# Kernel optimization log

Hardware: AMD Instinct MI355X
Metric: run time of the kernel (lower is better)

The kernel has to match this reference:

```python
import jax, jax.numpy as jnp
import numpy as np

B, T, C, H, K = 4, 2048, 2048, 32, 64
CHUNK = 64  # matches `splits = 64` in the torch source
EPS = 0.00064


def setup_inputs() -> dict:
    key = jax.random.key(0)
    ks = jax.random.split(key, 16)
    return {
        "x": jax.random.normal(ks[0], (B, T, C), jnp.float32),
        "state": jax.random.normal(ks[1], (1, 1, C), jnp.float32) * 0.1,
        "wkvstate": jax.random.normal(ks[2], (H, K, K), jnp.float32) * 0.02,
        "time_mix_k": jax.random.uniform(ks[3], (1, 1, C), jnp.float32),
        "time_mix_v": jax.random.uniform(ks[4], (1, 1, C), jnp.float32),
        "time_mix_r": jax.random.uniform(ks[5], (1, 1, C), jnp.float32),
        "time_mix_g": jax.random.uniform(ks[6], (1, 1, C), jnp.float32),
        "time_decay": jax.random.normal(ks[7], (H, K), jnp.float32) * 0.5,
        "time_faaaa": jax.random.normal(ks[8], (H, K), jnp.float32) * 0.1,
        "w_r": jax.random.normal(ks[9], (C, C), jnp.float32) * 0.02,
        "w_k": jax.random.normal(ks[10], (C, C), jnp.float32) * 0.02,
        "w_v": jax.random.normal(ks[11], (C, C), jnp.float32) * 0.02,
        "w_g": jax.random.normal(ks[12], (C, C), jnp.float32) * 0.02,
        "w_o": jax.random.normal(ks[13], (C, C), jnp.float32) * 0.02,
        "ln_w": jnp.ones((C,), jnp.float32),
        "ln_b": jnp.zeros((C,), jnp.float32),
    }


def reference(x, state, wkvstate, time_mix_k, time_mix_v, time_mix_r, time_mix_g,
              time_decay, time_faaaa, w_r, w_k, w_v, w_g, w_o, ln_w, ln_b):
    Bx, Tx, Cx = x.shape
    Hx, Kx = time_decay.shape

    # TimeShift (training path): prepend learned state, drop last token
    xx = jnp.concatenate([jnp.broadcast_to(state, (Bx, 1, Cx)), x[:, :-1]], axis=1)
    xk = x * time_mix_k + xx * (1.0 - time_mix_k)
    xv = x * time_mix_v + xx * (1.0 - time_mix_v)
    xr = x * time_mix_r + xx * (1.0 - time_mix_r)
    xg = x * time_mix_g + xx * (1.0 - time_mix_g)

    g = jax.nn.silu(xg @ w_g.T)  # (B,T,C)

    def to_heads(t):  # (B,T,C) -> (B,H,T,K)
        return t.reshape(Bx, Tx, Hx, Kx).transpose(0, 2, 1, 3)

    r = to_heads(xr @ w_r.T)
    k = to_heads(xk @ w_k.T)
    v = to_heads(xv @ w_v.T)

    w = jnp.exp(-jnp.exp(time_decay))  # (H,K), per-channel decay in (0,1)
    t_idx = jnp.arange(Tx)
    wfor = w[None, :, None, :] ** t_idx[None, None, :, None]          # w^t
    wback = w[None, :, None, :] ** (Tx - 1 - t_idx)[None, None, :, None]  # w^(T-1-t)

    # contribution of the incoming wkv state: (r * w^t) @ S0
    base = jnp.einsum('bhtk,hkj->bhtj', r * wfor, wkvstate)
    # bonus (u) diagonal term: sum_k(k_t * u * r_t) * v_t
    base = base + jnp.sum(k * r * time_faaaa[None, :, None, :], axis=-1, keepdims=True) * v

    kw = k * wback  # k_t scaled by w^(T-1-t), as in the source

    # strict-past causal product on shifted slices (r[:,1:] vs kw/v[:,:-1]),
    # computed chunk-by-chunk exactly like the blocked tril loop.
    rr, kk, vv = r[:, :, 1:], kw[:, :, :-1], v[:, :, :-1]
    Tm = Tx - 1
    pad = (-Tm) % CHUNK
    pd = lambda a: jnp.pad(a, ((0, 0), (0, 0), (0, pad), (0, 0)))
    rr, kk, vv = pd(rr), pd(kk), pd(vv)
    nC = (Tm + pad) // CHUNK
    resh = lambda a: a.reshape(Bx, Hx, nC, CHUNK, Kx).transpose(2, 0, 1, 3, 4)
    rc_, kc_, vc_ = resh(rr), resh(kk), resh(vv)
    mask = jnp.tril(jnp.ones((CHUNK, CHUNK), bool))  # q <= p (inclusive) == tril(i-j) globally

    def step(S, inp):
        rc, kc, vc = inp  # (B,H,CHUNK,K)
        att = jnp.einsum('bhpk,bhqk->bhpq', rc, kc)
        att = jnp.where(mask, att, 0.0)
        out = jnp.einsum('bhpq,bhqk->bhpk', att, vc) + jnp.einsum('bhpk,bhkj->bhpj', rc, S)
        S = S + jnp.einsum('bhqk,bhqj->bhkj', kc, vc)
        return S, out

    S0 = jnp.zeros((Bx, Hx, Kx, Kx), x.dtype)
    _, outs = jax.lax.scan(step, S0, (rc_, kc_, vc_))  # (nC,B,H,CHUNK,K)
    intra = outs.transpose(1, 2, 0, 3, 4).reshape(Bx, Hx, nC * CHUNK, Kx)[:, :, :Tm]
    wkv = base.at[:, :, 1:].add(intra)  # (B,H,T,K)

    # GroupNorm(n_head groups) after a bf16 round-trip, as in the source
    y = wkv.transpose(0, 2, 1, 3)  # (B,T,H,K)
    y = y.astype(jnp.bfloat16).astype(jnp.float32)
    mu = jnp.mean(y, axis=-1, keepdims=True)
    var = jnp.var(y, axis=-1, keepdims=True)
    y = (y - mu) / jnp.sqrt(var + EPS)
    y = y * ln_w.reshape(Hx, Kx) + ln_b.reshape(Hx, Kx)
    y = y.reshape(Bx, Tx, Cx)

    return (y * g) @ w_o.T
```

## Files before the change

kernel.cpp:

```cpp
#include <hip/hip_runtime.h>

#define Bn 4
#define Tn 2048
#define Cn 2048
#define Hn 32
#define Mn 8192
#define EPSV 0.00064f
#define SEGS 8
#define ZTHR 96.f

typedef __attribute__((ext_vector_type(8))) short short8;
typedef __attribute__((ext_vector_type(4))) float f32x4;
typedef _Float16 half4 __attribute__((ext_vector_type(4)));
typedef _Float16 half8 __attribute__((ext_vector_type(8)));

__device__ __forceinline__ unsigned short f2bf(float f) {
  unsigned int u = __float_as_uint(f);
  u += 0x7fffu + ((u >> 16) & 1u);
  return (unsigned short)(u >> 16);
}
__device__ __forceinline__ float bf2f(unsigned short h) {
  return __uint_as_float(((unsigned int)h) << 16);
}

__global__ __launch_bounds__(256) void wcast_f16_kernel(
    const float* __restrict__ src, _Float16* __restrict__ dst) {
  const size_t e = ((size_t)blockIdx.x * 256 + threadIdx.x) * 4;
  const float4 v = *(const float4*)(src + e);
  half4 h;
  h.x = (_Float16)v.x; h.y = (_Float16)v.y; h.z = (_Float16)v.z; h.w = (_Float16)v.w;
  *(half4*)(dst + e) = h;
}

__global__ __launch_bounds__(256) void mix_one_kernel(
    const float* __restrict__ x, const float* __restrict__ state,
    const float* __restrict__ tm, _Float16* __restrict__ xm) {
  const size_t e = ((size_t)blockIdx.x * 256 + threadIdx.x) * 4;
  const int c = (int)(e & (Cn - 1));
  const int t = (int)((e >> 11) & (Tn - 1));
  float4 xv  = *(const float4*)(x + e);
  float4 xxv = (t == 0) ? *(const float4*)(state + c) : *(const float4*)(x + e - Cn);
  float4 m = *(const float4*)(tm + c);
  half4 o;
  o.x = (_Float16)(xv.x * m.x + xxv.x * (1.f - m.x));
  o.y = (_Float16)(xv.y * m.y + xxv.y * (1.f - m.y));
  o.z = (_Float16)(xv.z * m.z + xxv.z * (1.f - m.z));
  o.w = (_Float16)(xv.w * m.w + xxv.w * (1.f - m.w));
  *(half4*)(xm + e) = o;
}

template <int OUT_F16>
__global__ __launch_bounds__(256) void gemm_f16_kernel(
    const _Float16* __restrict__ A, const _Float16* __restrict__ W,
    void* __restrict__ Ov) {
  __shared__ _Float16 As[128 * 32];
  __shared__ _Float16 Bs[128 * 32];
  const int tid = threadIdx.x;
  const int wv = tid >> 6, ln = tid & 63;
  const int wm = wv >> 1, wn = wv & 1;
  const int m16 = ln & 15, qd = ln >> 4;

  const _Float16* Ab = A + (size_t)blockIdx.y * 128 * Cn;
  const _Float16* Wb = W + (size_t)blockIdx.x * 128 * Cn;

  const _Float16* gA[2]; const _Float16* gB[2];
  int lof[2];
#pragma unroll
  for (int tc = 0; tc < 2; ++tc) {
    int lo = ((wv * 2 + tc) << 10);
    int r  = (lo >> 6) + (ln >> 2);
    int q  = (ln & 3) ^ ((r >> 1) & 3);
    gA[tc] = Ab + (size_t)r * Cn + (q << 3);
    gB[tc] = Wb + (size_t)r * Cn + (q << 3);
    lof[tc] = lo;
  }
  int aoff[4], boff[4];
#pragma unroll
  for (int mt = 0; mt < 4; ++mt) {
    int r = (wm << 6) + (mt << 4) + m16;
    aoff[mt] = (r << 6) + ((qd ^ ((r >> 1) & 3)) << 4);
  }
#pragma unroll
  for (int nt = 0; nt < 4; ++nt) {
    int r = (wn << 6) + (nt << 4) + m16;
    boff[nt] = (r << 6) + ((qd ^ ((r >> 1) & 3)) << 4);
  }

  f32x4 acc[4][4];
#pragma unroll
  for (int i = 0; i < 4; ++i)
#pragma unroll
    for (int j = 0; j < 4; ++j) acc[i][j] = 0.f;

  for (int k0 = 0; k0 < Cn; k0 += 32) {
#pragma unroll
    for (int tc = 0; tc < 2; ++tc) {
      __builtin_amdgcn_global_load_lds(
          (const __attribute__((address_space(1))) void*)(gA[tc] + k0),
          (__attribute__((address_space(3))) void*)((char*)As + lof[tc]), 16, 0, 0);
      __builtin_amdgcn_global_load_lds(
          (const __attribute__((address_space(1))) void*)(gB[tc] + k0),
          (__attribute__((address_space(3))) void*)((char*)Bs + lof[tc]), 16, 0, 0);
    }
    __syncthreads();
    half8 af[4], bfr[4];
#pragma unroll
    for (int mt = 0; mt < 4; ++mt) af[mt] = *(const half8*)((const char*)As + aoff[mt]);
#pragma unroll
    for (int nt = 0; nt < 4; ++nt) bfr[nt] = *(const half8*)((const char*)Bs + boff[nt]);
#pragma unroll
    for (int mt = 0; mt < 4; ++mt)
#pragma unroll
      for (int nt = 0; nt < 4; ++nt)
        acc[mt][nt] = __builtin_amdgcn_mfma_f32_16x16x32_f16(af[mt], bfr[nt], acc[mt][nt], 0, 0, 0);
    __syncthreads();
  }
#pragma unroll
  for (int mt = 0; mt < 4; ++mt) {
#pragma unroll
    for (int nt = 0; nt < 4; ++nt) {
      int col  = (wn << 6) + (nt << 4) + m16;
      int row0 = (wm << 6) + (mt << 4) + (qd << 2);
      f32x4 cv = acc[mt][nt];
      if constexpr (OUT_F16) {
        _Float16* Ob = (_Float16*)Ov + (size_t)blockIdx.y * 128 * Cn + (size_t)blockIdx.x * 128;
#pragma unroll
        for (int rg = 0; rg < 4; ++rg)
          Ob[(size_t)(row0 + rg) * Cn + col] = (_Float16)cv[rg];
      } else {
        float* Ob = (float*)Ov + (size_t)blockIdx.y * 128 * Cn + (size_t)blockIdx.x * 128;
#pragma unroll
        for (int rg = 0; rg < 4; ++rg)
          Ob[(size_t)(row0 + rg) * Cn + col] = cv[rg];
      }
    }
  }
}

__global__ __launch_bounds__(256) void seg_sum_kernel(
    const _Float16* __restrict__ kA, const _Float16* __restrict__ vA,
    const float* __restrict__ td, float* __restrict__ segsum) {
  __shared__ float sK[32][68];
  __shared__ float sV[32][68];
  __shared__ float sEw[64];
  __shared__ float sEwMin;
  const int tid = threadIdx.x;
  const int bh = blockIdx.x;
  const int seg = SEGS - 1 - blockIdx.y;
  const int b = bh >> 5, h = bh & 31;
  const size_t colbase = (size_t)b * Tn * Cn + h * 64;
  const _Float16* kG = kA + colbase;
  const _Float16* vG = vA + colbase;

  if (tid < 64) sEw[tid] = __expf(td[h * 64 + tid]);
  __syncthreads();
  if (tid == 0) {
    float mn = sEw[0];
    for (int i = 1; i < 64; ++i) mn = fminf(mn, sEw[i]);
    sEwMin = mn;
  }
  __syncthreads();

  const int uk0 = (tid >> 4) << 2;
  const int uj0 = (tid & 15) << 2;
  float su[16];
#pragma unroll
  for (int i = 0; i < 16; ++i) su[i] = 0.f;

  const int c0 = seg * (64 / SEGS), c1 = c0 + (64 / SEGS);
  for (int c = c0; c < c1; ++c) {
    const int tb = c << 5;
    if ((float)(Tn - 32 - tb) * sEwMin >= ZTHR) continue;
#pragma unroll
    for (int rep = 0; rep < 2; ++rep) {
      int f4 = tid + (rep << 8);
      int row = f4 >> 4;
      int col = (f4 & 15) << 2;
      int t = tb + row;
      size_t off = (size_t)t * Cn + col;
      half4 ku = *(const half4*)(kG + off);
      half4 vu = *(const half4*)(vG + off);
      float4 vf; vf.x = (float)vu.x; vf.y = (float)vu.y; vf.z = (float)vu.z; vf.w = (float)vu.w;
      *(float4*)&sV[row][col] = vf;
      float e = (float)(Tn - 1 - t);
      float4 kw;
      kw.x = (float)ku.x * __expf(-e * sEw[col + 0]);
      kw.y = (float)ku.y * __expf(-e * sEw[col + 1]);
      kw.z = (float)ku.z * __expf(-e * sEw[col + 2]);
      kw.w = (float)ku.w * __expf(-e * sEw[col + 3]);
      *(float4*)&sK[row][col] = kw;
    }
    __syncthreads();
    for (int q = 0; q < 32; ++q) {
      float4 kq = *(const float4*)&sK[q][uk0];
      float4 vq = *(const float4*)&sV[q][uj0];
      su[0]  += kq.x * vq.x; su[1]  += kq.x * vq.y; su[2]  += kq.x * vq.z; su[3]  += kq.x * vq.w;
      su[4]  += kq.y * vq.x; su[5]  += kq.y * vq.y; su[6]  += kq.y * vq.z; su[7]  += kq.y * vq.w;
      su[8]  += kq.z * vq.x; su[9]  += kq.z * vq.y; su[10] += kq.z * vq.z; su[11] += kq.z * vq.w;
      su[12] += kq.w * vq.x; su[13] += kq.w * vq.y; su[14] += kq.w * vq.z; su[15] += kq.w * vq.w;
    }
    __syncthreads();
  }
  float* dst = segsum + ((size_t)bh * SEGS + seg) * 4096;
#pragma unroll
  for (int i = 0; i < 4; ++i) {
    float4 s; s.x = su[i * 4 + 0]; s.y = su[i * 4 + 1]; s.z = su[i * 4 + 2]; s.w = su[i * 4 + 3];
    *(float4*)(dst + (uk0 + i) * 64 + uj0) = s;
  }
}

__global__ __launch_bounds__(256) void scan_kernel(
    const _Float16* __restrict__ rA, const _Float16* __restrict__ kA,
    const _Float16* __restrict__ vA, const _Float16* __restrict__ gA,
    const float* __restrict__ wkvst, const float* __restrict__ td,
    const float* __restrict__ faaaa, const float* __restrict__ lnw,
    const float* __restrict__ lnb, const float* __restrict__ segsum,
    _Float16* __restrict__ A2) {
  __shared__ float sR[32][68];
  __shared__ float sK[32][68];
  __shared__ float sV[32][68];
  __shared__ float sRW[32][68];
  __shared__ float sS[64][68];
  __shared__ float sS0[64][68];
  __shared__ float sAtt[32][36];
  __shared__ float sEw[64];
  __shared__ float sU[64];
  __shared__ float sDotP[32][16];
  __shared__ float sRedM[32][8];
  __shared__ float sRedQ[32][8];
  __shared__ float sMV[32][2];
  __shared__ float sEwMin;
  const int tid = threadIdx.x;
  const int bh = blockIdx.x;
  const int seg = SEGS - 1 - blockIdx.y;
  const int b = bh >> 5, h = bh & 31;
  const size_t colbase = (size_t)b * Tn * Cn + h * 64;
  const _Float16* rG = rA + colbase;
  const _Float16* kG = kA + colbase;
  const _Float16* vG = vA + colbase;
  const _Float16* gG = gA + colbase;
  _Float16* outG = A2 + colbase;

  if (tid < 64) {
    sEw[tid] = __expf(td[h * 64 + tid]);
    sU[tid]  = faaaa[h * 64 + tid];
  }
  {
    float4 acc4[4];
#pragma unroll
    for (int j = 0; j < 4; ++j) { acc4[j].x = 0.f; acc4[j].y = 0.f; acc4[j].z = 0.f; acc4[j].w = 0.f; }
    for (int sp = 0; sp < seg; ++sp) {
      const float* basep = segsum + ((size_t)bh * SEGS + sp) * 4096;
#pragma unroll
      for (int j = 0; j < 4; ++j) {
        int f4 = tid + j * 256;
        int row = f4 >> 4, c4 = (f4 & 15) << 2;
        float4 m = *(const float4*)(basep + row * 64 + c4);
        acc4[j].x += m.x; acc4[j].y += m.y; acc4[j].z += m.z; acc4[j].w += m.w;
      }
    }
#pragma unroll
    for (int j = 0; j < 4; ++j) {
      int f4 = tid + j * 256;
      int row = f4 >> 4, c4 = (f4 & 15) << 2;
      *(float4*)&sS[row][c4] = acc4[j];
      *(float4*)&sS0[row][c4] = *(const float4*)(wkvst + (size_t)h * 4096 + row * 64 + c4);
    }
  }
  __syncthreads();
  if (tid == 0) {
    float mn = sEw[0];
    for (int i = 1; i < 64; ++i) mn = fminf(mn, sEw[i]);
    sEwMin = mn;
  }
  __syncthreads();

  const int ap  = tid >> 3;
  const int aq0 = (tid & 7) << 2;
  const int oj0 = (tid & 7) << 3;
  const int uk0 = (tid >> 4) << 2;
  const int uj0 = (tid & 15) << 2;
  float lw[8], lb[8];
#pragma unroll
  for (int i = 0; i < 8; ++i) { lw[i] = lnw[h * 64 + oj0 + i]; lb[i] = lnb[h * 64 + oj0 + i]; }

  bool snz = (seg > 0) && ((float)(Tn - seg * 256) * sEwMin < ZTHR);

  const int c0 = seg * (64 / SEGS), c1 = c0 + (64 / SEGS);
  for (int c = c0; c < c1; ++c) {
    const int tb = c << 5;
    const bool skipc  = ((float)(Tn - 32 - tb) * sEwMin) >= ZTHR;
    const bool active = ((float)tb * sEwMin) < 88.f;
#pragma unroll
    for (int rep = 0; rep < 2; ++rep) {
      int f4 = tid + (rep << 8);
      int row = f4 >> 4;
      int col = (f4 & 15) << 2;
      int t = tb + row;
      size_t off = (size_t)t * Cn + col;
      half4 ru = *(const half4*)(rG + off);
      half4 ku = *(const half4*)(kG + off);
      half4 vu = *(const half4*)(vG + off);
      float4 rv; rv.x = (float)ru.x; rv.y = (float)ru.y; rv.z = (float)ru.z; rv.w = (float)ru.w;
      float4 kf; kf.x = (float)ku.x; kf.y = (float)ku.y; kf.z = (float)ku.z; kf.w = (float)ku.w;
      float4 vf; vf.x = (float)vu.x; vf.y = (float)vu.y; vf.z = (float)vu.z; vf.w = (float)vu.w;
      *(float4*)&sV[row][col] = vf;
      sDotP[row][f4 & 15] =
          kf.x * rv.x * sU[col + 0] + kf.y * rv.y * sU[col + 1] +
          kf.z * rv.z * sU[col + 2] + kf.w * rv.w * sU[col + 3];
      if (!skipc) {
        *(float4*)&sR[row][col] = rv;
        float e = (float)(Tn - 1 - t);
        float4 kw;
        kw.x = kf.x * __expf(-e * sEw[col + 0]); kw.y = kf.y * __expf(-e * sEw[col + 1]);
        kw.z = kf.z * __expf(-e * sEw[col + 2]); kw.w = kf.w * __expf(-e * sEw[col + 3]);
        *(float4*)&sK[row][col] = kw;
      }
      if (active) {
        float tt = (float)t;
        float4 rw;
        rw.x = rv.x * __expf(-tt * sEw[col + 0]); rw.y = rv.y * __expf(-tt * sEw[col + 1]);
        rw.z = rv.z * __expf(-tt * sEw[col + 2]); rw.w = rv.w * __expf(-tt * sEw[col + 3]);
        *(float4*)&sRW[row][col] = rw;
      }
    }
    __syncthreads();
    if (!skipc) {
      float a[4] = {0.f, 0.f, 0.f, 0.f};
      for (int k = 0; k < 64; k += 4) {
        float4 rv = *(const float4*)&sR[ap][k];
#pragma unroll
        for (int qq = 0; qq < 4; ++qq) {
          float4 kv = *(const float4*)&sK[aq0 + qq][k];
          a[qq] += rv.x * kv.x + rv.y * kv.y + rv.z * kv.z + rv.w * kv.w;
        }
      }
#pragma unroll
      for (int qq = 0; qq < 4; ++qq)
        sAtt[ap][aq0 + qq] = ((aq0 + qq) < ap) ? a[qq] : 0.f;
      __syncthreads();
    }
    float y[8];
    {
      float o[8];
#pragma unroll
      for (int i = 0; i < 8; ++i) o[i] = 0.f;
      if (!skipc) {
        for (int q = 0; q < 32; ++q) {
          float aw = sAtt[ap][q];
          float4 v0 = *(const float4*)&sV[q][oj0];
          float4 v1 = *(const float4*)&sV[q][oj0 + 4];
          o[0] += aw * v0.x; o[1] += aw * v0.y; o[2] += aw * v0.z; o[3] += aw * v0.w;
          o[4] += aw * v1.x; o[5] += aw * v1.y; o[6] += aw * v1.z; o[7] += aw * v1.w;
        }
      }
      if (snz) {
        for (int k = 0; k < 64; ++k) {
          float rw = sR[ap][k];
          float4 s0 = *(const float4*)&sS[k][oj0];
          float4 s1 = *(const float4*)&sS[k][oj0 + 4];
          o[0] += rw * s0.x; o[1] += rw * s0.y; o[2] += rw * s0.z; o[3] += rw * s0.w;
          o[4] += rw * s1.x; o[5] += rw * s1.y; o[6] += rw * s1.z; o[7] += rw * s1.w;
        }
      }
      if (active) {
        for (int k = 0; k < 64; ++k) {
          float rw = sRW[ap][k];
          float4 s0 = *(const float4*)&sS0[k][oj0];
          float4 s1 = *(const float4*)&sS0[k][oj0 + 4];
          o[0] += rw * s0.x; o[1] += rw * s0.y; o[2] += rw * s0.z; o[3] += rw * s0.w;
          o[4] += rw * s1.x; o[5] += rw * s1.y; o[6] += rw * s1.z; o[7] += rw * s1.w;
        }
      }
      float dot = 0.f;
#pragma unroll
      for (int s = 0; s < 16; ++s) dot += sDotP[ap][s];
#pragma unroll
      for (int i = 0; i < 8; ++i) o[i] += dot * sV[ap][oj0 + i];
      float sm = 0.f, sq = 0.f;
#pragma unroll
      for (int i = 0; i < 8; ++i) {
        y[i] = bf2f(f2bf(o[i]));
        sm += y[i]; sq += y[i] * y[i];
      }
      sRedM[ap][tid & 7] = sm; sRedQ[ap][tid & 7] = sq;
    }
    __syncthreads();
    if ((tid & 7) == 0) {
      float sm = 0.f, sq = 0.f;
#pragma unroll
      for (int i = 0; i < 8; ++i) { sm += sRedM[ap][i]; sq += sRedQ[ap][i]; }
      float mu = sm * (1.f / 64.f);
      float var = sq * (1.f / 64.f) - mu * mu;
      sMV[ap][0] = mu; sMV[ap][1] = rsqrtf(var + EPSV);
    }
    __syncthreads();
    {
      float mu = sMV[ap][0], rs = sMV[ap][1];
      int t = tb + ap;
      size_t off = (size_t)t * Cn + oj0;
      half4 g0 = *(const half4*)(gG + off);
      half4 g1 = *(const half4*)(gG + off + 4);
      float gv[8] = {(float)g0.x, (float)g0.y, (float)g0.z, (float)g0.w,
                     (float)g1.x, (float)g1.y, (float)g1.z, (float)g1.w};
      _Float16 us[8];
#pragma unroll
      for (int i = 0; i < 8; ++i) {
        float yn = (y[i] - mu) * rs * lw[i] + lb[i];
        float gs = gv[i] / (1.f + __expf(-gv[i]));
        us[i] = (_Float16)(yn * gs);
      }
      half4 o0, o1;
      o0.x = us[0]; o0.y = us[1]; o0.z = us[2]; o0.w = us[3];
      o1.x = us[4]; o1.y = us[5]; o1.z = us[6]; o1.w = us[7];
      *(half4*)(outG + off) = o0;
      *(half4*)(outG + off + 4) = o1;
    }
    if (!skipc) {
      float su[16];
#pragma unroll
      for (int i = 0; i < 4; ++i) {
        float4 s = *(const float4*)&sS[uk0 + i][uj0];
        su[i * 4 + 0] = s.x; su[i * 4 + 1] = s.y; su[i * 4 + 2] = s.z; su[i * 4 + 3] = s.w;
      }
      for (int q = 0; q < 32; ++q) {
        float4 kq = *(const float4*)&sK[q][uk0];
        float4 vq = *(const float4*)&sV[q][uj0];
        su[0]  += kq.x * vq.x; su[1]  += kq.x * vq.y; su[2]  += kq.x * vq.z; su[3]  += kq.x * vq.w;
        su[4]  += kq.y * vq.x; su[5]  += kq.y * vq.y; su[6]  += kq.y * vq.z; su[7]  += kq.y * vq.w;
        su[8]  += kq.z * vq.x; su[9]  += kq.z * vq.y; su[10] += kq.z * vq.z; su[11] += kq.z * vq.w;
        su[12] += kq.w * vq.x; su[13] += kq.w * vq.y; su[14] += kq.w * vq.z; su[15] += kq.w * vq.w;
      }
#pragma unroll
      for (int i = 0; i < 4; ++i) {
        float4 s; s.x = su[i * 4 + 0]; s.y = su[i * 4 + 1]; s.z = su[i * 4 + 2]; s.w = su[i * 4 + 3];
        *(float4*)&sS[uk0 + i][uj0] = s;
      }
      snz = true;
      __syncthreads();
    }
  }
}

extern "C" void kernel_launch(void* const* d_in, const int* in_sizes, int n_in,
                              void* d_out, int out_size, void* d_ws, size_t ws_size,
                              hipStream_t stream) {
  const float* x     = (const float*)d_in[0];
  const float* state = (const float*)d_in[1];
  const float* wkvst = (const float*)d_in[2];
  const float* tmk   = (const float*)d_in[3];
  const float* tmv   = (const float*)d_in[4];
  const float* tmr   = (const float*)d_in[5];
  const float* tmg   = (const float*)d_in[6];
  const float* td    = (const float*)d_in[7];
  const float* faaaa = (const float*)d_in[8];
  const float* w_r   = (const float*)d_in[9];
  const float* w_k   = (const float*)d_in[10];
  const float* w_v   = (const float*)d_in[11];
  const float* w_g   = (const float*)d_in[12];
  const float* w_o   = (const float*)d_in[13];
  const float* ln_w  = (const float*)d_in[14];
  const float* ln_b  = (const float*)d_in[15];
  float* out = (float*)d_out;
  char* ws = (char*)d_ws;

  _Float16* wh  = (_Float16*)(ws);
  _Float16* xm  = (_Float16*)(ws + 16777216);
  _Float16* A2  = (_Float16*)(ws + 16777216);
  _Float16* proj = (_Float16*)(ws + 50331648);
  float* segsum  = (float*)(ws + 184549376);
  const size_t SLOT_E = (size_t)Mn * Cn;
  _Float16* R = proj;
  _Float16* K = proj + SLOT_E;
  _Float16* V = proj + 2 * SLOT_E;
  _Float16* G = proj + 3 * SLOT_E;

  const float* tms[4]  = {tmr, tmk, tmv, tmg};
  const float* wsrc[4] = {w_r, w_k, w_v, w_g};
  _Float16*    pdst[4] = {R, K, V, G};

  for (int s = 0; s < 4; ++s) {
    wcast_f16_kernel<<<dim3(4096), 256, 0, stream>>>(wsrc[s], wh);
    mix_one_kernel<<<dim3(16384), 256, 0, stream>>>(x, state, tms[s], xm);
    gemm_f16_kernel<1><<<dim3(16, 64), 256, 0, stream>>>(xm, wh, pdst[s]);
  }

  seg_sum_kernel<<<dim3(128, SEGS), 256, 0, stream>>>(K, V, td, segsum);
  scan_kernel<<<dim3(128, SEGS), 256, 0, stream>>>(R, K, V, G, wkvst, td, faaaa,
                                                   ln_w, ln_b, segsum, A2);

  wcast_f16_kernel<<<dim3(4096), 256, 0, stream>>>(w_o, wh);
  gemm_f16_kernel<0><<<dim3(16, 64), 256, 0, stream>>>(A2, wh, out);

  (void)in_sizes; (void)n_in; (void)out_size; (void)ws_size;
}
```

Baseline: 907.0 us.

## Replace 128x128 GEMM with double-buffered 256x256x64 tiled MFMA kernel

The projection and output GEMMs move from a single-buffered 128x128 tile with K-step 32 and 256 threads to a 256x256 tile with K-step 64, 512 threads and double-buffered LDS. The next K-slice is loaded directly into LDS with an explicit vmcnt wait before each barrier, and s_setprio wraps the MFMA bursts. Larger tiles cut global traffic per FLOP and the prefetch is meant to hide load latency behind compute. The cost is 128KB of LDS per block and high accumulator register pressure, and the 256-block grid leaves exactly one block per CU.

```diff
diff --git a/kernel.cpp b/kernel.cpp
--- a/kernel.cpp
+++ b/kernel.cpp
@@ -9,7 +9,6 @@
 #define SEGS 8
 #define ZTHR 96.f
 
-typedef __attribute__((ext_vector_type(8))) short short8;
 typedef __attribute__((ext_vector_type(4))) float f32x4;
 typedef _Float16 half4 __attribute__((ext_vector_type(4)));
 typedef _Float16 half8 __attribute__((ext_vector_type(8)));
@@ -50,85 +49,120 @@
 }
 
 template <int OUT_F16>
-__global__ __launch_bounds__(256) void gemm_f16_kernel(
+__global__ __launch_bounds__(512, 2) void gemm256_kernel(
     const _Float16* __restrict__ A, const _Float16* __restrict__ W,
     void* __restrict__ Ov) {
-  __shared__ _Float16 As[128 * 32];
-  __shared__ _Float16 Bs[128 * 32];
+  __shared__ _Float16 As[2][256 * 64];
+  __shared__ _Float16 Bs[2][256 * 64];
   const int tid = threadIdx.x;
-  const int wv = tid >> 6, ln = tid & 63;
-  const int wm = wv >> 1, wn = wv & 1;
+  const int wid = tid >> 6, ln = tid & 63;
+  const int wm = wid >> 2, wn = wid & 3;
   const int m16 = ln & 15, qd = ln >> 4;
 
-  const _Float16* Ab = A + (size_t)blockIdx.y * 128 * Cn;
-  const _Float16* Wb = W + (size_t)blockIdx.x * 128 * Cn;
-
-  const _Float16* gA[2]; const _Float16* gB[2];
-  int lof[2];
-#pragma unroll
-  for (int tc = 0; tc < 2; ++tc) {
-    int lo = ((wv * 2 + tc) << 10);
-    int r  = (lo >> 6) + (ln >> 2);
-    int q  = (ln & 3) ^ ((r >> 1) & 3);
-    gA[tc] = Ab + (size_t)r * Cn + (q << 3);
-    gB[tc] = Wb + (size_t)r * Cn + (q << 3);
-    lof[tc] = lo;
-  }
-  int aoff[4], boff[4];
-#pragma unroll
-  for (int mt = 0; mt < 4; ++mt) {
-    int r = (wm << 6) + (mt << 4) + m16;
-    aoff[mt] = (r << 6) + ((qd ^ ((r >> 1) & 3)) << 4);
-  }
-#pragma unroll
-  for (int nt = 0; nt < 4; ++nt) {
-    int r = (wn << 6) + (nt << 4) + m16;
-    boff[nt] = (r << 6) + ((qd ^ ((r >> 1) & 3)) << 4);
-  }
-
-  f32x4 acc[4][4];
-#pragma unroll
-  for (int i = 0; i < 4; ++i)
+  const int mtile = blockIdx.y, ntile = blockIdx.x;
+  const _Float16* Ab = A + (size_t)mtile * 256 * Cn;
+  const _Float16* Wb = W + (size_t)ntile * 256 * Cn;
+
+  const _Float16* gA[4]; const _Float16* gB[4];
+  int lof[4];
+#pragma unroll
+  for (int i = 0; i < 4; ++i) {
+    int r = ((wid * 4 + i) << 3) + (ln >> 3);
+    int q = (ln & 7) ^ (r & 7);
+    gA[i] = Ab + (size_t)r * Cn + (q << 3);
+    gB[i] = Wb + (size_t)r * Cn + (q << 3);
+    lof[i] = ((wid * 4 + i) << 10);
+  }
+  int aob[2], bob[2];
+#pragma unroll
+  for (int h = 0; h < 2; ++h) {
+    int sl = ((h << 2) + qd) ^ (m16 & 7);
+    aob[h] = (wm * 128 + m16) * 128 + sl * 16;
+    bob[h] = (wn * 64 + m16) * 128 + sl * 16;
+  }
+
+  f32x4 acc[8][4];
+#pragma unroll
+  for (int i = 0; i < 8; ++i)
 #pragma unroll
     for (int j = 0; j < 4; ++j) acc[i][j] = 0.f;
 
-  for (int k0 = 0; k0 < Cn; k0 += 32) {
-#pragma unroll
-    for (int tc = 0; tc < 2; ++tc) {
-      __builtin_amdgcn_global_load_lds(
-          (const __attribute__((address_space(1))) void*)(gA[tc] + k0),
-          (__attribute__((address_space(3))) void*)((char*)As + lof[tc]), 16, 0, 0);
-      __builtin_amdgcn_global_load_lds(
-          (const __attribute__((address_space(1))) void*)(gB[tc] + k0),
-          (__attribute__((address_space(3))) void*)((char*)Bs + lof[tc]), 16, 0, 0);
-    }
-    __syncthreads();
-    half8 af[4], bfr[4];
-#pragma unroll
-    for (int mt = 0; mt < 4; ++mt) af[mt] = *(const half8*)((const char*)As + aoff[mt]);
-#pragma unroll
-    for (int nt = 0; nt < 4; ++nt) bfr[nt] = *(const half8*)((const char*)Bs + boff[nt]);
-#pragma unroll
-    for (int mt = 0; mt < 4; ++mt)
-#pragma unroll
-      for (int nt = 0; nt < 4; ++nt)
-        acc[mt][nt] = __builtin_amdgcn_mfma_f32_16x16x32_f16(af[mt], bfr[nt], acc[mt][nt], 0, 0, 0);
-    __syncthreads();
-  }
-#pragma unroll
-  for (int mt = 0; mt < 4; ++mt) {
-#pragma unroll
-    for (int nt = 0; nt < 4; ++nt) {
-      int col  = (wn << 6) + (nt << 4) + m16;
-      int row0 = (wm << 6) + (mt << 4) + (qd << 2);
-      f32x4 cv = acc[mt][nt];
+#pragma unroll
+  for (int i = 0; i < 4; ++i) {
+    __builtin_amdgcn_global_load_lds(
+        (const __attribute__((address_space(1))) void*)(gA[i]),
+        (__attribute__((address_space(3))) void*)((char*)&As[0][0] + lof[i]), 16, 0, 0);
+    __builtin_amdgcn_global_load_lds(
+        (const __attribute__((address_space(1))) void*)(gB[i]),
+        (__attribute__((address_space(3))) void*)((char*)&Bs[0][0] + lof[i]), 16, 0, 0);
+  }
+
+  const int NT = Cn / 64;
+  for (int t = 0; t < NT; ++t) {
+    const int b = t & 1;
+    if (t + 1 < NT) {
+      const int k0 = (t + 1) << 6;
+#pragma unroll
+      for (int i = 0; i < 4; ++i) {
+        __builtin_amdgcn_global_load_lds(
+            (const __attribute__((address_space(1))) void*)(gA[i] + k0),
+            (__attribute__((address_space(3))) void*)((char*)&As[b ^ 1][0] + lof[i]), 16, 0, 0);
+        __builtin_amdgcn_global_load_lds(
+            (const __attribute__((address_space(1))) void*)(gB[i] + k0),
+            (__attribute__((address_space(3))) void*)((char*)&Bs[b ^ 1][0] + lof[i]), 16, 0, 0);
+      }
+      asm volatile("s_waitcnt vmcnt(8)" ::: "memory");
+    } else {
+      asm volatile("s_waitcnt vmcnt(0)" ::: "memory");
+    }
+    __builtin_amdgcn_s_barrier();
+
+    const char* Abase = (const char*)&As[b][0];
+    const char* Bbase = (const char*)&Bs[b][0];
+    half8 bf[4][2];
+#pragma unroll
+    for (int nf = 0; nf < 4; ++nf)
+#pragma unroll
+      for (int h = 0; h < 2; ++h)
+        bf[nf][h] = *(const half8*)(Bbase + nf * 2048 + bob[h]);
+#pragma unroll
+    for (int p = 0; p < 4; ++p) {
+      half8 af[2][2];
+#pragma unroll
+      for (int sub = 0; sub < 2; ++sub)
+#pragma unroll
+        for (int h = 0; h < 2; ++h)
+          af[sub][h] = *(const half8*)(Abase + (p * 2 + sub) * 2048 + aob[h]);
+      __builtin_amdgcn_s_setprio(1);
+#pragma unroll
+      for (int sub = 0; sub < 2; ++sub)
+#pragma unroll
+        for (int nf = 0; nf < 4; ++nf) {
+          acc[p * 2 + sub][nf] =
+              __builtin_amdgcn_mfma_f32_16x16x32_f16(af[sub][0], bf[nf][0], acc[p * 2 + sub][nf], 0, 0, 0);
+          acc[p * 2 + sub][nf] =
+              __builtin_amdgcn_mfma_f32_16x16x32_f16(af[sub][1], bf[nf][1], acc[p * 2 + sub][nf], 0, 0, 0);
+        }
+      __builtin_amdgcn_s_setprio(0);
+    }
+    __builtin_amdgcn_s_barrier();
+  }
+
+  const size_t obase = (size_t)mtile * 256 * Cn + (size_t)ntile * 256;
+#pragma unroll
+  for (int fr = 0; fr < 8; ++fr) {
+#pragma unroll
+    for (int nf = 0; nf < 4; ++nf) {
+      int col  = wn * 64 + nf * 16 + m16;
+      int row0 = wm * 128 + fr * 16 + (qd << 2);
+      f32x4 cv = acc[fr][nf];
       if constexpr (OUT_F16) {
-        _Float16* Ob = (_Float16*)Ov + (size_t)blockIdx.y * 128 * Cn + (size_t)blockIdx.x * 128;
+        _Float16* Ob = (_Float16*)Ov + obase;
 #pragma unroll
         for (int rg = 0; rg < 4; ++rg)
           Ob[(size_t)(row0 + rg) * Cn + col] = (_Float16)cv[rg];
       } else {
-        float* Ob = (float*)Ov + (size_t)blockIdx.y * 128 * Cn + (size_t)blockIdx.x * 128;
+        float* Ob = (float*)Ov + obase;
 #pragma unroll
         for (int rg = 0; rg < 4; ++rg)
           Ob[(size_t)(row0 + rg) * Cn + col] = cv[rg];
@@ -482,7 +516,7 @@
   for (int s = 0; s < 4; ++s) {
     wcast_f16_kernel<<<dim3(4096), 256, 0, stream>>>(wsrc[s], wh);
     mix_one_kernel<<<dim3(16384), 256, 0, stream>>>(x, state, tms[s], xm);
-    gemm_f16_kernel<1><<<dim3(16, 64), 256, 0, stream>>>(xm, wh, pdst[s]);
+    gemm256_kernel<1><<<dim3(Cn / 256, Mn / 256), 512, 0, stream>>>(xm, wh, pdst[s]);
   }
 
   seg_sum_kernel<<<dim3(128, SEGS), 256, 0, stream>>>(K, V, td, segsum);
@@ -490,7 +524,7 @@
                                                    ln_w, ln_b, segsum, A2);
 
   wcast_f16_kernel<<<dim3(4096), 256, 0, stream>>>(w_o, wh);
-  gemm_f16_kernel<0><<<dim3(16, 64), 256, 0, stream>>>(A2, wh, out);
+  gemm256_kernel<0><<<dim3(Cn / 256, Mn / 256), 512, 0, stream>>>(A2, wh, out);
 
   (void)in_sizes; (void)n_in; (void)out_size; (void)ws_size;
 }
```

After: 769.1 us. -15.2%, faster.
